# Optimization experiments

Hardware: AMD Instinct MI355X
Metric: run time of the kernel (lower is better)

## Reference

```python
import jax, jax.numpy as jnp
import numpy as np

BATCH = 32
N_LEVELS = (16384, 4096, 1024, 256)   # nodes at each mesh resolution
M_LEVELS = (4096, 1024, 256, 64)      # nodes after each Pool (downsample)
DEG = 6                               # directed edges per node
POOL_K = 3                            # nnz per row of downsample matrix
FILTERS = (3, 32, 32, 32, 64)         # channel chain of the 4 ChebConvs
K_CHEB = 6                            # Chebyshev polynomial order


def setup_inputs() -> dict:
    key = jax.random.key(0)
    ks = iter(jax.random.split(key, 64))
    inp = {"x": jax.random.normal(next(ks), (BATCH, N_LEVELS[0], FILTERS[0]), jnp.float32)}
    for i, N in enumerate(N_LEVELS):
        er = jnp.repeat(jnp.arange(N), DEG)
        off = jax.random.randint(next(ks), (N * DEG,), 1, N)
        inp[f"er{i}"] = er
        inp[f"ec{i}"] = (er + off) % N  # guaranteed no self loops
    for i, (M, N) in enumerate(zip(M_LEVELS, N_LEVELS)):
        inp[f"pr{i}"] = jnp.repeat(jnp.arange(M), POOL_K)
        inp[f"pc{i}"] = jax.random.randint(next(ks), (M * POOL_K,), 0, N)
        inp[f"pv{i}"] = jax.random.uniform(next(ks), (M * POOL_K,), jnp.float32)
    for i in range(4):
        fin, fout = FILTERS[i], FILTERS[i + 1]
        scale = 1.0 / np.sqrt(fin * K_CHEB)
        inp[f"W{i}"] = jax.random.normal(next(ks), (K_CHEB, fin, fout), jnp.float32) * scale
        inp[f"b{i}"] = jnp.zeros((fout,), jnp.float32)
    inp["enc_W"] = jax.random.normal(next(ks), (M_LEVELS[-1] * FILTERS[-1], 128), jnp.float32) * 0.1
    inp["enc_b"] = jnp.zeros((128,), jnp.float32)
    inp["cls_W"] = jax.random.normal(next(ks), (128, 10), jnp.float32) * 0.1
    inp["cls_b"] = jnp.zeros((10,), jnp.float32)
    return inp


def _cheb_conv(x, er, ec, W, b):
    # x: [B,N,Fin]; W: [K,Fin,Fout].
    # PyG ChebConv with lambda_max=2: L_hat = L - I = -D^{-1/2} A D^{-1/2}.
    N = x.shape[1]
    deg = jnp.zeros((N,), x.dtype).at[er].add(1.0)
    dinv = jnp.where(deg > 0, 1.0 / jnp.sqrt(jnp.maximum(deg, 1.0)), 0.0)
    norm = -(dinv[er] * dinv[ec])  # [E]

    def L(t):  # sparse matvec: gather neighbor feats, weight, scatter-add
        return jnp.zeros_like(t).at[:, er].add(t[:, ec] * norm[None, :, None])

    Tx0 = x
    out = jnp.einsum("bnf,fg->bng", Tx0, W[0])
    Tx1 = L(x)
    out = out + jnp.einsum("bnf,fg->bng", Tx1, W[1])
    for k in range(2, W.shape[0]):
        Tx2 = 2.0 * L(Tx1) - Tx0
        out = out + jnp.einsum("bnf,fg->bng", Tx2, W[k])
        Tx0, Tx1 = Tx1, Tx2
    return out + b


def _pool(x, pr, pc, pv, m):
    # sparse downsample matrix [m,N]: index_select cols * value, scatter_add rows
    B, _, F = x.shape
    return jnp.zeros((B, m, F), x.dtype).at[:, pr].add(x[:, pc] * pv[None, :, None])


def reference(x, er0, ec0, er1, ec1, er2, ec2, er3, ec3,
              pr0, pc0, pv0, pr1, pc1, pv1, pr2, pc2, pv2, pr3, pc3, pv3,
              W0, b0, W1, b1, W2, b2, W3, b3, enc_W, enc_b, cls_W, cls_b):
    ers, ecs = (er0, er1, er2, er3), (ec0, ec1, ec2, ec3)
    prs, pcs, pvs = (pr0, pr1, pr2, pr3), (pc0, pc1, pc2, pc3), (pv0, pv1, pv2, pv3)
    Ws, bs = (W0, W1, W2, W3), (b0, b1, b2, b3)
    for i in range(4):  # fixed n_layers loop (structurally distinct layers)
        x = jax.nn.relu(_cheb_conv(x, ers[i], ecs[i], Ws[i], bs[i]))
        x = _pool(x, prs[i], pcs[i], pvs[i], M_LEVELS[i])
    x = x.reshape(x.shape[0], -1)  # [B, 64*64]
    h = jax.nn.relu(x @ enc_W + enc_b)
    return h @ cls_W + cls_b
```

## Files before the change

### kernel.cpp

```cpp
#include <hip/hip_runtime.h>
#include <hip/hip_fp16.h>
#include <cstddef>
#include <cstdint>

#define BATCH 32


struct alignas(8) half4 { __half2 lo, hi; };

__device__ __forceinline__ void h4f(const half4 h, float f[4]) {
  float2 a = __half22float2(h.lo);
  float2 c = __half22float2(h.hi);
  f[0] = a.x; f[1] = a.y; f[2] = c.x; f[3] = c.y;
}
__device__ __forceinline__ void fma4(float4& a, float s, const float4& w) {
  a.x += s * w.x; a.y += s * w.y; a.z += s * w.z; a.w += s * w.w;
}
__device__ __forceinline__ float4 relu4(const float4& a) {
  return make_float4(fmaxf(a.x, 0.f), fmaxf(a.y, 0.f), fmaxf(a.z, 0.f), fmaxf(a.w, 0.f));
}

__global__ void __launch_bounds__(1024, 4) cheb_chain0(
    const float* __restrict__ x,
    const int* __restrict__ ec,
    __half* __restrict__ Th)
{
  __shared__ half4 cur[16384];
  const int b = blockIdx.x;
  const float cI = -1.0f / 6.0f;
  const float cS = -1.0f / 3.0f;
  half4 prevv[16];
  half4 newh[16];

#pragma unroll
  for (int i = 0; i < 16; ++i) {
    int n = threadIdx.x + (i << 10);
    const float* src = x + ((size_t)b * 16384 + n) * 3;
    half4 h;
    h.lo = __floats2half2_rn(src[0], src[1]);
    h.hi = __floats2half2_rn(src[2], 0.f);
    cur[n] = h;
  }
  __syncthreads();

#pragma unroll 1
  for (int k = 1; k <= 5; ++k) {
    half4* Tk = (half4*)Th + (size_t)(k - 1) * 524288 + (size_t)b * 16384;
#pragma unroll
    for (int i = 0; i < 16; ++i) {
      int n = threadIdx.x + (i << 10);
      const int2* e2 = (const int2*)(ec + n * 6);
      int2 ea = e2[0], eb = e2[1], ez = e2[2];
      int na[6];
      na[0] = ea.x; na[1] = ea.y; na[2] = eb.x;
      na[3] = eb.y; na[4] = ez.x; na[5] = ez.y;
      float s0 = 0.f, s1 = 0.f, s2 = 0.f;
#pragma unroll
      for (int d = 0; d < 6; ++d) {
        half4 t = cur[na[d]];
        float2 a = __half22float2(t.lo);
        float2 c = __half22float2(t.hi);
        s0 += a.x; s1 += a.y; s2 += c.x;
      }
      float v0, v1, v2;
      if (k == 1) {
        v0 = cI * s0; v1 = cI * s1; v2 = cI * s2;
      } else {
        float2 pa = __half22float2(prevv[i].lo);
        float2 pc = __half22float2(prevv[i].hi);
        v0 = cS * s0 - pa.x; v1 = cS * s1 - pa.y; v2 = cS * s2 - pc.x;
      }
      half4 h;
      h.lo = __floats2half2_rn(v0, v1);
      h.hi = __floats2half2_rn(v2, 0.f);
      newh[i] = h;
      Tk[n] = h;
    }
    __syncthreads();
#pragma unroll
    for (int i = 0; i < 16; ++i) {
      int n = threadIdx.x + (i << 10);
      prevv[i] = cur[n];
      cur[n] = newh[i];
    }
    __syncthreads();
  }
}

__global__ void __launch_bounds__(256) pool_conv_f3_bm(
    const float* __restrict__ x, const half4* __restrict__ T,
    const float* __restrict__ W, const float* __restrict__ bias,
    const int* __restrict__ pc, const float* __restrict__ pv,
    float* __restrict__ out)
{
  constexpr int FOUT = 32;
  constexpr int F4 = FOUT / 4;
  __shared__ float Ws[6 * 3 * FOUT];
  for (int i = threadIdx.x; i < 6 * 3 * FOUT; i += 256) Ws[i] = W[i];
  __syncthreads();
  const float4* Ws4 = (const float4*)Ws;
  int t = blockIdx.x * 256 + threadIdx.x;
  int fo4 = t % F4;
  int b   = (t / F4) % BATCH;
  int m   = t / (F4 * BATCH);
  int c0 = pc[m * 3 + 0], c1 = pc[m * 3 + 1], c2 = pc[m * 3 + 2];
  float v0 = pv[m * 3 + 0], v1 = pv[m * 3 + 1], v2 = pv[m * 3 + 2];
  float4 bi = ((const float4*)bias)[fo4];
  float4 a0 = bi, a1 = bi, a2 = bi;
  {
    const float* x0 = x + ((size_t)b * 16384 + c0) * 3;
    const float* x1 = x + ((size_t)b * 16384 + c1) * 3;
    const float* x2 = x + ((size_t)b * 16384 + c2) * 3;
#pragma unroll
    for (int f = 0; f < 3; ++f) {
      float4 w = Ws4[f * F4 + fo4];
      fma4(a0, x0[f], w);
      fma4(a1, x1[f], w);
      fma4(a2, x2[f], w);
    }
  }
#pragma unroll
  for (int k = 1; k < 6; ++k) {
    const half4* base = T + (size_t)(k - 1) * 524288 + (size_t)b * 16384;
    float r0[4], r1[4], r2[4];
    h4f(base[c0], r0);
    h4f(base[c1], r1);
    h4f(base[c2], r2);
#pragma unroll
    for (int f = 0; f < 3; ++f) {
      float4 w = Ws4[(k * 3 + f) * F4 + fo4];
      fma4(a0, r0[f], w);
      fma4(a1, r1[f], w);
      fma4(a2, r2[f], w);
    }
  }
  a0 = relu4(a0); a1 = relu4(a1); a2 = relu4(a2);
  float4 acc;
  acc.x = v0*a0.x + v1*a1.x + v2*a2.x;
  acc.y = v0*a0.y + v1*a1.y + v2*a2.y;
  acc.z = v0*a0.z + v1*a1.z + v2*a2.z;
  acc.w = v0*a0.w + v1*a1.w + v2*a2.w;
  ((float4*)out)[((size_t)m * BATCH + b) * F4 + fo4] = acc;
}

template<int N, int F, int THREADS, int MINW>
__global__ void __launch_bounds__(THREADS, MINW) cheb_recur_hh(
    const float* __restrict__ X,
    const int* __restrict__ ec,
    __half* __restrict__ Th)
{
  constexpr int NPT = N / THREADS;
  __shared__ half4 cur[N];
  const float cI = -1.0f / 6.0f;
  const float cS = -1.0f / 3.0f;
  const int b = blockIdx.x & 31;
  const int fbase = (blockIdx.x >> 5) * 4;
  constexpr size_t SLH = (size_t)N * 32 * F;
  half4 prevv[NPT];
  half4 newh[NPT];
#pragma unroll
  for (int i = 0; i < NPT; ++i) {
    int n = threadIdx.x + i * THREADS;
    float4 xv = *(const float4*)(X + ((size_t)n * 32 + b) * F + fbase);
    half4 h;
    h.lo = __floats2half2_rn(xv.x, xv.y);
    h.hi = __floats2half2_rn(xv.z, xv.w);
    cur[n] = h;
  }
  __syncthreads();
#pragma unroll 1
  for (int k = 1; k <= 5; ++k) {
    __half* Tk = Th + (size_t)(k - 1) * SLH;
#pragma unroll
    for (int i = 0; i < NPT; ++i) {
      int n = threadIdx.x + i * THREADS;
      const int2* e2 = (const int2*)(ec + n * 6);
      int2 ea = e2[0], eb = e2[1], ez = e2[2];
      int na[6];
      na[0] = ea.x; na[1] = ea.y; na[2] = eb.x;
      na[3] = eb.y; na[4] = ez.x; na[5] = ez.y;
      float s0 = 0.f, s1 = 0.f, s2 = 0.f, s3 = 0.f;
#pragma unroll
      for (int d = 0; d < 6; ++d) {
        half4 t = cur[na[d]];
        float2 a = __half22float2(t.lo);
        float2 c = __half22float2(t.hi);
        s0 += a.x; s1 += a.y; s2 += c.x; s3 += c.y;
      }
      float v0, v1, v2, v3;
      if (k == 1) {
        v0 = cI * s0; v1 = cI * s1; v2 = cI * s2; v3 = cI * s3;
      } else {
        float2 pa = __half22float2(prevv[i].lo);
        float2 pc = __half22float2(prevv[i].hi);
        v0 = cS * s0 - pa.x; v1 = cS * s1 - pa.y;
        v2 = cS * s2 - pc.x; v3 = cS * s3 - pc.y;
      }
      half4 h;
      h.lo = __floats2half2_rn(v0, v1);
      h.hi = __floats2half2_rn(v2, v3);
      newh[i] = h;
      *(half4*)(Tk + ((size_t)n * 32 + b) * F + fbase) = h;
    }
    __syncthreads();
#pragma unroll
    for (int i = 0; i < NPT; ++i) {
      int n = threadIdx.x + i * THREADS;
      prevv[i] = cur[n];
      cur[n] = newh[i];
    }
    __syncthreads();
  }
}

template<int N, int M, int FOUT, bool OUT_BM>
__global__ void __launch_bounds__(256) pool_conv_v32_h(
    const float* __restrict__ X, const __half* __restrict__ Th,
    const float* __restrict__ W, const float* __restrict__ bias,
    const int* __restrict__ pc, const float* __restrict__ pv,
    float* __restrict__ out)
{
  constexpr int FIN = 32;
  constexpr int F4 = FOUT / 4;
  constexpr size_t SLH = (size_t)N * 32 * FIN;
  __shared__ float Ws[6 * FIN * FOUT];
  for (int i = threadIdx.x; i < 6 * FIN * FOUT; i += 256) Ws[i] = W[i];
  __syncthreads();
  const float4* Ws4 = (const float4*)Ws;
  const float4* X4p = (const float4*)X;
  int t = blockIdx.x * 256 + threadIdx.x;
  int fo4 = t % F4;
  int b   = (t / F4) % BATCH;
  int m   = t / (F4 * BATCH);
  int c0 = pc[m * 3 + 0], c1 = pc[m * 3 + 1], c2 = pc[m * 3 + 2];
  float v0 = pv[m * 3 + 0], v1 = pv[m * 3 + 1], v2 = pv[m * 3 + 2];
  float4 bi = ((const float4*)bias)[fo4];
  float4 a0 = bi, a1 = bi, a2 = bi;
  {
    const float4* r0 = X4p + ((size_t)c0 * BATCH + b) * 8;
    const float4* r1 = X4p + ((size_t)c1 * BATCH + b) * 8;
    const float4* r2 = X4p + ((size_t)c2 * BATCH + b) * 8;
#pragma unroll
    for (int fi = 0; fi < 8; ++fi) {
      float4 t0 = r0[fi], t1 = r1[fi], t2 = r2[fi];
#pragma unroll
      for (int ff = 0; ff < 4; ++ff) {
        float4 w = Ws4[(fi * 4 + ff) * F4 + fo4];
        fma4(a0, ((const float*)&t0)[ff], w);
        fma4(a1, ((const float*)&t1)[ff], w);
        fma4(a2, ((const float*)&t2)[ff], w);
      }
    }
  }
#pragma unroll 1
  for (int k = 1; k < 6; ++k) {
    const half4* base = (const half4*)(Th + (size_t)(k - 1) * SLH);
    const half4* r0 = base + ((size_t)c0 * 32 + b) * 8;
    const half4* r1 = base + ((size_t)c1 * 32 + b) * 8;
    const half4* r2 = base + ((size_t)c2 * 32 + b) * 8;
#pragma unroll
    for (int q = 0; q < 8; ++q) {
      float f0[4], f1[4], f2[4];
      h4f(r0[q], f0); h4f(r1[q], f1); h4f(r2[q], f2);
#pragma unroll
      for (int ff = 0; ff < 4; ++ff) {
        float4 w = Ws4[((k * 32) + q * 4 + ff) * F4 + fo4];
        fma4(a0, f0[ff], w);
        fma4(a1, f1[ff], w);
        fma4(a2, f2[ff], w);
      }
    }
  }
  a0 = relu4(a0); a1 = relu4(a1); a2 = relu4(a2);
  float4 acc;
  acc.x = v0*a0.x + v1*a1.x + v2*a2.x;
  acc.y = v0*a0.y + v1*a1.y + v2*a2.y;
  acc.z = v0*a0.z + v1*a1.z + v2*a2.z;
  acc.w = v0*a0.w + v1*a1.w + v2*a2.w;
  size_t oi = OUT_BM ? (((size_t)b * M + m) * F4 + fo4) : (((size_t)m * BATCH + b) * F4 + fo4);
  ((float4*)out)[oi] = acc;
}

__global__ void __launch_bounds__(256) encoder_partial(
    const float* __restrict__ Xf, const float* __restrict__ encW,
    float* __restrict__ partial)
{
  int b  = blockIdx.x;
  int ks = blockIdx.y;
  int fo = threadIdx.x & 127;
  int half = threadIdx.x >> 7;
  const float* xr = Xf + b * 4096 + ks * 256 + half * 128;
  const float* w  = encW + (size_t)(ks * 256 + half * 128) * 128;
  float acc = 0.f;
#pragma unroll 8
  for (int i = 0; i < 128; ++i) acc += xr[i] * w[(size_t)i * 128 + fo];
  __shared__ float part[256];
  part[threadIdx.x] = acc;
  __syncthreads();
  if (half == 0) partial[(size_t)(b * 16 + ks) * 128 + fo] = part[fo] + part[128 + fo];
}

__global__ void __launch_bounds__(128) encoder_reduce_cls(
    const float* __restrict__ partial, const float* __restrict__ encB,
    const float* __restrict__ clsW, const float* __restrict__ clsB,
    float* __restrict__ out)
{
  int b = blockIdx.x;
  int fo = threadIdx.x;
  float acc = encB[fo];
#pragma unroll
  for (int ks = 0; ks < 16; ++ks) acc += partial[(size_t)(b * 16 + ks) * 128 + fo];
  __shared__ float Hs[128];
  Hs[fo] = fmaxf(acc, 0.f);
  __syncthreads();
  if (fo < 10) {
    float s = clsB[fo];
#pragma unroll 4
    for (int f = 0; f < 128; ++f) s += Hs[f] * clsW[f * 10 + fo];
    out[b * 10 + fo] = s;
  }
}

extern "C" void kernel_launch(void* const* d_in, const int* in_sizes, int n_in,
                              void* d_out, int out_size, void* d_ws, size_t ws_size,
                              hipStream_t stream)
{
  const float* x   = (const float*)d_in[0];
  const int* ec0 = (const int*)d_in[2];
  const int* ec1 = (const int*)d_in[4];
  const int* ec2 = (const int*)d_in[6];
  const int* ec3 = (const int*)d_in[8];
  const int* pc0 = (const int*)d_in[10]; const float* pv0 = (const float*)d_in[11];
  const int* pc1 = (const int*)d_in[13]; const float* pv1 = (const float*)d_in[14];
  const int* pc2 = (const int*)d_in[16]; const float* pv2 = (const float*)d_in[17];
  const int* pc3 = (const int*)d_in[19]; const float* pv3 = (const float*)d_in[20];
  const float* W0 = (const float*)d_in[21]; const float* b0 = (const float*)d_in[22];
  const float* W1 = (const float*)d_in[23]; const float* b1 = (const float*)d_in[24];
  const float* W2 = (const float*)d_in[25]; const float* b2 = (const float*)d_in[26];
  const float* W3 = (const float*)d_in[27]; const float* b3 = (const float*)d_in[28];
  const float* encW = (const float*)d_in[29]; const float* encB = (const float*)d_in[30];
  const float* clsW = (const float*)d_in[31]; const float* clsB = (const float*)d_in[32];
  float* out = (float*)d_out;

  float* ws = (float*)d_ws;
  __half* Th = (__half*)ws;
  float* X1 = ws + 10485760;
  float* X2 = X1 + 4194304;
  float* X3 = X2 + 1048576;
  float* X4 = X3 + 262144;
  float* P  = X4 + 131072;

  dim3 blk(256);

  cheb_chain0<<<dim3(32), dim3(1024), 0, stream>>>(x, ec0, Th);
  pool_conv_f3_bm<<<dim3(4096), blk, 0, stream>>>(
      x, (const half4*)Th, W0, b0, pc0, pv0, X1);

  cheb_recur_hh<4096, 32, 1024, 4><<<dim3(256), dim3(1024), 0, stream>>>(X1, ec1, Th);
  pool_conv_v32_h<4096, 1024, 32, false><<<dim3(1024), blk, 0, stream>>>(
      X1, Th, W1, b1, pc1, pv1, X2);

  cheb_recur_hh<1024, 32, 256, 4><<<dim3(256), blk, 0, stream>>>(X2, ec2, Th);
  pool_conv_v32_h<1024, 256, 32, false><<<dim3(256), blk, 0, stream>>>(
      X2, Th, W2, b2, pc2, pv2, X3);

  cheb_recur_hh<256, 32, 256, 4><<<dim3(256), blk, 0, stream>>>(X3, ec3, Th);
  pool_conv_v32_h<256, 64, 64, true><<<dim3(128), blk, 0, stream>>>(
      X3, Th, W3, b3, pc3, pv3, X4);

  encoder_partial<<<dim3(32, 16), blk, 0, stream>>>(X4, encW, P);
  encoder_reduce_cls<<<dim3(32), dim3(128), 0, stream>>>(P, encB, clsW, clsB, out);
}
```

Before: 346.4 us.

## Fuse whole network into cooperative mega-kernel and spread level-0 recurrence across grid

Replaces the chain of separate launches with a single cooperative kernel that uses grid-wide syncs between stages. The level-0 Chebyshev recurrence, previously run by 32 blocks in shared memory, is now distributed over all blocks with a node-major half-precision layout in global memory. The aim is to remove launch gaps and the low parallelism of the first layer. In exchange it adds grid-sync overhead and global-memory round trips between recurrence steps, and falls back to multi-kernel launches if the cooperative launch fails.

After: 726.1 us. 2.1x slower.

```diff
diff --git a/kernel.cpp b/kernel.cpp
--- a/kernel.cpp
+++ b/kernel.cpp
@@ -1,7 +1,10 @@
 #include <hip/hip_runtime.h>
 #include <hip/hip_fp16.h>
+#include <hip/hip_cooperative_groups.h>
 #include <cstddef>
 #include <cstdint>
+
+namespace cg = cooperative_groups;
 
 #define BATCH 32
 
@@ -20,86 +23,99 @@
   return make_float4(fmaxf(a.x, 0.f), fmaxf(a.y, 0.f), fmaxf(a.z, 0.f), fmaxf(a.w, 0.f));
 }
 
-__global__ void __launch_bounds__(1024, 4) cheb_chain0(
-    const float* __restrict__ x,
-    const int* __restrict__ ec,
-    __half* __restrict__ Th)
-{
-  __shared__ half4 cur[16384];
-  const int b = blockIdx.x;
-  const float cI = -1.0f / 6.0f;
-  const float cS = -1.0f / 3.0f;
-  half4 prevv[16];
-  half4 newh[16];
-
-#pragma unroll
-  for (int i = 0; i < 16; ++i) {
-    int n = threadIdx.x + (i << 10);
-    const float* src = x + ((size_t)b * 16384 + n) * 3;
-    half4 h;
-    h.lo = __floats2half2_rn(src[0], src[1]);
-    h.hi = __floats2half2_rn(src[2], 0.f);
-    cur[n] = h;
-  }
-  __syncthreads();
-
-#pragma unroll 1
-  for (int k = 1; k <= 5; ++k) {
-    half4* Tk = (half4*)Th + (size_t)(k - 1) * 524288 + (size_t)b * 16384;
-#pragma unroll
-    for (int i = 0; i < 16; ++i) {
-      int n = threadIdx.x + (i << 10);
-      const int2* e2 = (const int2*)(ec + n * 6);
-      int2 ea = e2[0], eb = e2[1], ez = e2[2];
-      int na[6];
-      na[0] = ea.x; na[1] = ea.y; na[2] = eb.x;
-      na[3] = eb.y; na[4] = ez.x; na[5] = ez.y;
-      float s0 = 0.f, s1 = 0.f, s2 = 0.f;
-#pragma unroll
-      for (int d = 0; d < 6; ++d) {
-        half4 t = cur[na[d]];
-        float2 a = __half22float2(t.lo);
-        float2 c = __half22float2(t.hi);
-        s0 += a.x; s1 += a.y; s2 += c.x;
-      }
-      float v0, v1, v2;
-      if (k == 1) {
-        v0 = cI * s0; v1 = cI * s1; v2 = cI * s2;
-      } else {
-        float2 pa = __half22float2(prevv[i].lo);
-        float2 pc = __half22float2(prevv[i].hi);
-        v0 = cS * s0 - pa.x; v1 = cS * s1 - pa.y; v2 = cS * s2 - pc.x;
-      }
-      half4 h;
-      h.lo = __floats2half2_rn(v0, v1);
-      h.hi = __floats2half2_rn(v2, 0.f);
-      newh[i] = h;
-      Tk[n] = h;
-    }
-    __syncthreads();
-#pragma unroll
-    for (int i = 0; i < 16; ++i) {
-      int n = threadIdx.x + (i << 10);
-      prevv[i] = cur[n];
-      cur[n] = newh[i];
-    }
-    __syncthreads();
-  }
-}
-
-__global__ void __launch_bounds__(256) pool_conv_f3_bm(
-    const float* __restrict__ x, const half4* __restrict__ T,
-    const float* __restrict__ W, const float* __restrict__ bias,
+
+__device__ __forceinline__ void d_transpose_cell(
+    const float* __restrict__ x, half4* __restrict__ xh, int t)
+{
+  int n = t >> 5;
+  int b = t & 31;
+  const float* src = x + ((size_t)b * 16384 + n) * 3;
+  half4 h;
+  h.lo = __floats2half2_rn(src[0], src[1]);
+  h.hi = __floats2half2_rn(src[2], 0.f);
+  xh[t] = h;
+}
+
+__device__ __forceinline__ void d_cheb_cell(
+    const half4* __restrict__ Tin, const half4* __restrict__ Tpp,
+    const int* __restrict__ ec, half4* __restrict__ Tout,
+    float coef, float beta, int idx)
+{
+  int n = idx >> 5;
+  const int2* e2 = (const int2*)(ec + n * 6);
+  int2 ea = e2[0], eb = e2[1], ez = e2[2];
+  int na[6];
+  na[0] = ea.x; na[1] = ea.y; na[2] = eb.x;
+  na[3] = eb.y; na[4] = ez.x; na[5] = ez.y;
+  int b = idx & 31;
+  float s0 = 0.f, s1 = 0.f, s2 = 0.f;
+#pragma unroll
+  for (int d = 0; d < 6; ++d) {
+    half4 v = Tin[(na[d] << 5) | b];
+    float2 a = __half22float2(v.lo);
+    float2 c = __half22float2(v.hi);
+    s0 += a.x; s1 += a.y; s2 += c.x;
+  }
+  half4 p = Tpp[idx];
+  float2 pa = __half22float2(p.lo);
+  float2 pc = __half22float2(p.hi);
+  half4 o;
+  o.lo = __floats2half2_rn(coef * s0 + beta * pa.x, coef * s1 + beta * pa.y);
+  o.hi = __floats2half2_rn(coef * s2 + beta * pc.x, 0.f);
+  Tout[idx] = o;
+}
+
+__device__ __forceinline__ void d_poolf3_cell(
+    const half4* __restrict__ Xh, const half4* __restrict__ T,
+    const float* __restrict__ Ws, const float* __restrict__ bias,
     const int* __restrict__ pc, const float* __restrict__ pv,
-    float* __restrict__ out)
-{
-  constexpr int FOUT = 32;
+    float* __restrict__ out, int t)
+{
+  constexpr int F4 = 8;
+  constexpr size_t SL = (size_t)16384 * 32;
+  const float4* Ws4 = (const float4*)Ws;
+  int fo4 = t % F4;
+  int b   = (t / F4) % BATCH;
+  int m   = t / (F4 * BATCH);
+  int c0 = pc[m * 3 + 0], c1 = pc[m * 3 + 1], c2 = pc[m * 3 + 2];
+  float v0 = pv[m * 3 + 0], v1 = pv[m * 3 + 1], v2 = pv[m * 3 + 2];
+  float4 bi = ((const float4*)bias)[fo4];
+  float4 a0 = bi, a1 = bi, a2 = bi;
+#pragma unroll
+  for (int k = 0; k < 6; ++k) {
+    const half4* base = (k == 0) ? Xh : (T + (size_t)(k - 1) * SL);
+    float r0[4], r1[4], r2[4];
+    h4f(base[(c0 << 5) | b], r0);
+    h4f(base[(c1 << 5) | b], r1);
+    h4f(base[(c2 << 5) | b], r2);
+#pragma unroll
+    for (int f = 0; f < 3; ++f) {
+      float4 w = Ws4[(k * 3 + f) * F4 + fo4];
+      fma4(a0, r0[f], w);
+      fma4(a1, r1[f], w);
+      fma4(a2, r2[f], w);
+    }
+  }
+  a0 = relu4(a0); a1 = relu4(a1); a2 = relu4(a2);
+  float4 acc;
+  acc.x = v0*a0.x + v1*a1.x + v2*a2.x;
+  acc.y = v0*a0.y + v1*a1.y + v2*a2.y;
+  acc.z = v0*a0.z + v1*a1.z + v2*a2.z;
+  acc.w = v0*a0.w + v1*a1.w + v2*a2.w;
+  ((float4*)out)[((size_t)m * BATCH + b) * F4 + fo4] = acc;
+}
+
+template<int N, int M, int FOUT, bool OUT_BM>
+__device__ __forceinline__ void d_pool32_cell(
+    const float* __restrict__ X, const __half* __restrict__ Th,
+    const float* __restrict__ Ws, const float* __restrict__ bias,
+    const int* __restrict__ pc, const float* __restrict__ pv,
+    float* __restrict__ out, int t)
+{
   constexpr int F4 = FOUT / 4;
-  __shared__ float Ws[6 * 3 * FOUT];
-  for (int i = threadIdx.x; i < 6 * 3 * FOUT; i += 256) Ws[i] = W[i];
-  __syncthreads();
+  constexpr size_t SLH = (size_t)N * 32 * 32;
   const float4* Ws4 = (const float4*)Ws;
-  int t = blockIdx.x * 256 + threadIdx.x;
+  const float4* X4p = (const float4*)X;
   int fo4 = t % F4;
   int b   = (t / F4) % BATCH;
   int m   = t / (F4 * BATCH);
@@ -108,30 +124,38 @@
   float4 bi = ((const float4*)bias)[fo4];
   float4 a0 = bi, a1 = bi, a2 = bi;
   {
-    const float* x0 = x + ((size_t)b * 16384 + c0) * 3;
-    const float* x1 = x + ((size_t)b * 16384 + c1) * 3;
-    const float* x2 = x + ((size_t)b * 16384 + c2) * 3;
-#pragma unroll
-    for (int f = 0; f < 3; ++f) {
-      float4 w = Ws4[f * F4 + fo4];
-      fma4(a0, x0[f], w);
-      fma4(a1, x1[f], w);
-      fma4(a2, x2[f], w);
-    }
-  }
-#pragma unroll
+    const float4* r0 = X4p + ((size_t)c0 * BATCH + b) * 8;
+    const float4* r1 = X4p + ((size_t)c1 * BATCH + b) * 8;
+    const float4* r2 = X4p + ((size_t)c2 * BATCH + b) * 8;
+#pragma unroll
+    for (int fi = 0; fi < 8; ++fi) {
+      float4 t0 = r0[fi], t1 = r1[fi], t2 = r2[fi];
+#pragma unroll
+      for (int ff = 0; ff < 4; ++ff) {
+        float4 w = Ws4[(fi * 4 + ff) * F4 + fo4];
+        fma4(a0, ((const float*)&t0)[ff], w);
+        fma4(a1, ((const float*)&t1)[ff], w);
+        fma4(a2, ((const float*)&t2)[ff], w);
+      }
+    }
+  }
+#pragma unroll 1
   for (int k = 1; k < 6; ++k) {
-    const half4* base = T + (size_t)(k - 1) * 524288 + (size_t)b * 16384;
-    float r0[4], r1[4], r2[4];
-    h4f(base[c0], r0);
-    h4f(base[c1], r1);
-    h4f(base[c2], r2);
-#pragma unroll
-    for (int f = 0; f < 3; ++f) {
-      float4 w = Ws4[(k * 3 + f) * F4 + fo4];
-      fma4(a0, r0[f], w);
-      fma4(a1, r1[f], w);
-      fma4(a2, r2[f], w);
+    const half4* base = (const half4*)(Th + (size_t)(k - 1) * SLH);
+    const half4* r0 = base + ((size_t)c0 * 32 + b) * 8;
+    const half4* r1 = base + ((size_t)c1 * 32 + b) * 8;
+    const half4* r2 = base + ((size_t)c2 * 32 + b) * 8;
+#pragma unroll
+    for (int q = 0; q < 8; ++q) {
+      float f0[4], f1[4], f2[4];
+      h4f(r0[q], f0); h4f(r1[q], f1); h4f(r2[q], f2);
+#pragma unroll
+      for (int ff = 0; ff < 4; ++ff) {
+        float4 w = Ws4[((k * 32) + q * 4 + ff) * F4 + fo4];
+        fma4(a0, f0[ff], w);
+        fma4(a1, f1[ff], w);
+        fma4(a2, f2[ff], w);
+      }
     }
   }
   a0 = relu4(a0); a1 = relu4(a1); a2 = relu4(a2);
@@ -140,13 +164,240 @@
   acc.y = v0*a0.y + v1*a1.y + v2*a2.y;
   acc.z = v0*a0.z + v1*a1.z + v2*a2.z;
   acc.w = v0*a0.w + v1*a1.w + v2*a2.w;
-  ((float4*)out)[((size_t)m * BATCH + b) * F4 + fo4] = acc;
+  size_t oi = OUT_BM ? (((size_t)b * M + m) * F4 + fo4) : (((size_t)m * BATCH + b) * F4 + fo4);
+  ((float4*)out)[oi] = acc;
+}
+
+template<int N, int NPT>
+__device__ void d_recur_stage(
+    const float* __restrict__ X, const int* __restrict__ ec,
+    __half* __restrict__ Th, half4* cur, int bid, int tid)
+{
+  const float cI = -1.0f / 6.0f;
+  const float cS = -1.0f / 3.0f;
+  const int b = bid & 31;
+  const int fbase = (bid >> 5) * 4;
+  constexpr size_t SLH = (size_t)N * 32 * 32;
+  half4 prevv[NPT], newh[NPT];
+#pragma unroll
+  for (int i = 0; i < NPT; ++i) {
+    int n = tid + i * 512;
+    if (n < N) {
+      float4 xv = *(const float4*)(X + ((size_t)n * 32 + b) * 32 + fbase);
+      half4 h;
+      h.lo = __floats2half2_rn(xv.x, xv.y);
+      h.hi = __floats2half2_rn(xv.z, xv.w);
+      cur[n] = h;
+    }
+  }
+  __syncthreads();
+#pragma unroll 1
+  for (int k = 1; k <= 5; ++k) {
+    __half* Tk = Th + (size_t)(k - 1) * SLH;
+#pragma unroll
+    for (int i = 0; i < NPT; ++i) {
+      int n = tid + i * 512;
+      if (n < N) {
+        const int2* e2 = (const int2*)(ec + n * 6);
+        int2 ea = e2[0], eb = e2[1], ez = e2[2];
+        int na[6];
+        na[0] = ea.x; na[1] = ea.y; na[2] = eb.x;
+        na[3] = eb.y; na[4] = ez.x; na[5] = ez.y;
+        float s0 = 0.f, s1 = 0.f, s2 = 0.f, s3 = 0.f;
+#pragma unroll
+        for (int d = 0; d < 6; ++d) {
+          half4 t = cur[na[d]];
+          float2 a = __half22float2(t.lo);
+          float2 c = __half22float2(t.hi);
+          s0 += a.x; s1 += a.y; s2 += c.x; s3 += c.y;
+        }
+        float v0, v1, v2, v3;
+        if (k == 1) {
+          v0 = cI * s0; v1 = cI * s1; v2 = cI * s2; v3 = cI * s3;
+        } else {
+          float2 pa = __half22float2(prevv[i].lo);
+          float2 pc = __half22float2(prevv[i].hi);
+          v0 = cS * s0 - pa.x; v1 = cS * s1 - pa.y;
+          v2 = cS * s2 - pc.x; v3 = cS * s3 - pc.y;
+        }
+        half4 h;
+        h.lo = __floats2half2_rn(v0, v1);
+        h.hi = __floats2half2_rn(v2, v3);
+        newh[i] = h;
+        *(half4*)(Tk + ((size_t)n * 32 + b) * 32 + fbase) = h;
+      }
+    }
+    __syncthreads();
+#pragma unroll
+    for (int i = 0; i < NPT; ++i) {
+      int n = tid + i * 512;
+      if (n < N) {
+        prevv[i] = cur[n];
+        cur[n] = newh[i];
+      }
+    }
+    __syncthreads();
+  }
+}
+
+
+struct MegaP {
+  const float* x;
+  const int *ec0, *ec1, *ec2, *ec3;
+  const int *pc0, *pc1, *pc2, *pc3;
+  const float *pv0, *pv1, *pv2, *pv3;
+  const float *W0, *b0, *W1, *b1, *W2, *b2, *W3, *b3;
+  const float *encW, *encB, *clsW, *clsB;
+  float* out;
+  half4* Xh; __half* Th;
+  float *X1, *X2, *X3, *X4, *P;
+};
+
+__global__ void __launch_bounds__(512, 2) mega(MegaP P)
+{
+  cg::grid_group grid = cg::this_grid();
+  __shared__ __align__(16) char smemraw[49152];
+  half4* scur = (half4*)smemraw;
+  float* sws  = (float*)smemraw;
+  const int bid = blockIdx.x;
+  const int tid = threadIdx.x;
+  const float cI = -1.0f / 6.0f;
+  const float cS = -1.0f / 3.0f;
+
+#pragma unroll
+  for (int u = 0; u < 4; ++u)
+    d_transpose_cell(P.x, P.Xh, u * 131072 + bid * 512 + tid);
+  grid.sync();
+
+  {
+    const size_t S = (size_t)16384 * 32;
+    half4* T4 = (half4*)P.Th;
+    const half4* Tin[5] = { P.Xh, T4, T4 + S, T4 + 2*S, T4 + 3*S };
+    const half4* Tpp[5] = { P.Xh, P.Xh, T4, T4 + S, T4 + 2*S };
+    half4* Tout[5]      = { T4, T4 + S, T4 + 2*S, T4 + 3*S, T4 + 4*S };
+#pragma unroll 1
+    for (int k = 0; k < 5; ++k) {
+      float coef = (k == 0) ? cI : cS;
+      float beta = (k == 0) ? 0.f : -1.f;
+#pragma unroll
+      for (int u = 0; u < 4; ++u)
+        d_cheb_cell(Tin[k], Tpp[k], P.ec0, Tout[k], coef, beta,
+                    u * 131072 + bid * 512 + tid);
+      grid.sync();
+    }
+  }
+
+  for (int i = tid; i < 6 * 3 * 32; i += 512) sws[i] = P.W0[i];
+  __syncthreads();
+#pragma unroll 1
+  for (int u = 0; u < 8; ++u)
+    d_poolf3_cell(P.Xh, (const half4*)P.Th, sws, P.b0, P.pc0, P.pv0, P.X1,
+                  u * 131072 + bid * 512 + tid);
+  grid.sync();
+
+  d_recur_stage<4096, 8>(P.X1, P.ec1, P.Th, scur, bid, tid);
+  grid.sync();
+
+  for (int i = tid; i < 6 * 32 * 32; i += 512) sws[i] = P.W1[i];
+  __syncthreads();
+#pragma unroll 1
+  for (int u = 0; u < 2; ++u)
+    d_pool32_cell<4096, 1024, 32, false>(P.X1, P.Th, sws, P.b1, P.pc1, P.pv1,
+                                         P.X2, u * 131072 + bid * 512 + tid);
+  grid.sync();
+
+  d_recur_stage<1024, 2>(P.X2, P.ec2, P.Th, scur, bid, tid);
+  grid.sync();
+
+  for (int i = tid; i < 6 * 32 * 32; i += 512) sws[i] = P.W2[i];
+  __syncthreads();
+  {
+    int t = bid * 512 + tid;
+    if (t < 65536)
+      d_pool32_cell<1024, 256, 32, false>(P.X2, P.Th, sws, P.b2, P.pc2, P.pv2,
+                                          P.X3, t);
+  }
+  grid.sync();
+
+  d_recur_stage<256, 1>(P.X3, P.ec3, P.Th, scur, bid, tid);
+  grid.sync();
+
+  for (int i = tid; i < 6 * 32 * 64; i += 512) sws[i] = P.W3[i];
+  __syncthreads();
+  {
+    int t = bid * 512 + tid;
+    if (t < 32768)
+      d_pool32_cell<256, 64, 64, true>(P.X3, P.Th, sws, P.b3, P.pc3, P.pv3,
+                                       P.X4, t);
+  }
+  grid.sync();
+
+  {
+    int t = bid * 512 + tid;
+    if (t < 65536) {
+      int fo = t & 127;
+      int ks = (t >> 7) & 15;
+      int b  = t >> 11;
+      const float* xr = P.X4 + b * 4096 + ks * 256;
+      const float* w  = P.encW + (size_t)(ks * 256) * 128 + fo;
+      float acc = 0.f;
+#pragma unroll 8
+      for (int i = 0; i < 256; ++i) acc += xr[i] * w[(size_t)i * 128];
+      P.P[(size_t)(b * 16 + ks) * 128 + fo] = acc;
+    }
+  }
+  grid.sync();
+
+  if (bid < 32) {
+    int b = bid;
+    float* hs = sws;
+    if (tid < 128) {
+      float acc = P.encB[tid];
+#pragma unroll
+      for (int ks = 0; ks < 16; ++ks)
+        acc += P.P[(size_t)(b * 16 + ks) * 128 + tid];
+      hs[tid] = fmaxf(acc, 0.f);
+    }
+    __syncthreads();
+    if (tid < 10) {
+      float s = P.clsB[tid];
+#pragma unroll 4
+      for (int f = 0; f < 128; ++f) s += hs[f] * P.clsW[f * 10 + tid];
+      P.out[b * 10 + tid] = s;
+    }
+  }
+}
+
+
+__global__ void __launch_bounds__(256) transpose_h(
+    const float* __restrict__ x, half4* __restrict__ xh)
+{
+  d_transpose_cell(x, xh, blockIdx.x * 256 + threadIdx.x);
+}
+
+__global__ void __launch_bounds__(256) cheb_step_h(
+    const half4* __restrict__ Tin, const half4* __restrict__ Tpp,
+    const int* __restrict__ ec, half4* __restrict__ Tout,
+    float coef, float beta)
+{
+  d_cheb_cell(Tin, Tpp, ec, Tout, coef, beta, blockIdx.x * 256 + threadIdx.x);
+}
+
+__global__ void __launch_bounds__(256) pool_conv_f3_h(
+    const half4* __restrict__ Xh, const half4* __restrict__ T,
+    const float* __restrict__ W, const float* __restrict__ bias,
+    const int* __restrict__ pc, const float* __restrict__ pv,
+    float* __restrict__ out)
+{
+  __shared__ float Ws[6 * 3 * 32];
+  for (int i = threadIdx.x; i < 6 * 3 * 32; i += 256) Ws[i] = W[i];
+  __syncthreads();
+  d_poolf3_cell(Xh, T, Ws, bias, pc, pv, out, blockIdx.x * 256 + threadIdx.x);
 }
 
 template<int N, int F, int THREADS, int MINW>
 __global__ void __launch_bounds__(THREADS, MINW) cheb_recur_hh(
-    const float* __restrict__ X,
-    const int* __restrict__ ec,
+    const float* __restrict__ X, const int* __restrict__ ec,
     __half* __restrict__ Th)
 {
   constexpr int NPT = N / THREADS;
@@ -156,8 +407,7 @@
   const int b = blockIdx.x & 31;
   const int fbase = (blockIdx.x >> 5) * 4;
   constexpr size_t SLH = (size_t)N * 32 * F;
-  half4 prevv[NPT];
-  half4 newh[NPT];
+  half4 prevv[NPT], newh[NPT];
 #pragma unroll
   for (int i = 0; i < NPT; ++i) {
     int n = threadIdx.x + i * THREADS;
@@ -220,65 +470,11 @@
     const int* __restrict__ pc, const float* __restrict__ pv,
     float* __restrict__ out)
 {
-  constexpr int FIN = 32;
-  constexpr int F4 = FOUT / 4;
-  constexpr size_t SLH = (size_t)N * 32 * FIN;
-  __shared__ float Ws[6 * FIN * FOUT];
-  for (int i = threadIdx.x; i < 6 * FIN * FOUT; i += 256) Ws[i] = W[i];
-  __syncthreads();
-  const float4* Ws4 = (const float4*)Ws;
-  const float4* X4p = (const float4*)X;
-  int t = blockIdx.x * 256 + threadIdx.x;
-  int fo4 = t % F4;
-  int b   = (t / F4) % BATCH;
-  int m   = t / (F4 * BATCH);
-  int c0 = pc[m * 3 + 0], c1 = pc[m * 3 + 1], c2 = pc[m * 3 + 2];
-  float v0 = pv[m * 3 + 0], v1 = pv[m * 3 + 1], v2 = pv[m * 3 + 2];
-  float4 bi = ((const float4*)bias)[fo4];
-  float4 a0 = bi, a1 = bi, a2 = bi;
-  {
-    const float4* r0 = X4p + ((size_t)c0 * BATCH + b) * 8;
-    const float4* r1 = X4p + ((size_t)c1 * BATCH + b) * 8;
-    const float4* r2 = X4p + ((size_t)c2 * BATCH + b) * 8;
-#pragma unroll
-    for (int fi = 0; fi < 8; ++fi) {
-      float4 t0 = r0[fi], t1 = r1[fi], t2 = r2[fi];
-#pragma unroll
-      for (int ff = 0; ff < 4; ++ff) {
-        float4 w = Ws4[(fi * 4 + ff) * F4 + fo4];
-        fma4(a0, ((const float*)&t0)[ff], w);
-        fma4(a1, ((const float*)&t1)[ff], w);
-        fma4(a2, ((const float*)&t2)[ff], w);
-      }
-    }
-  }
-#pragma unroll 1
-  for (int k = 1; k < 6; ++k) {
-    const half4* base = (const half4*)(Th + (size_t)(k - 1) * SLH);
-    const half4* r0 = base + ((size_t)c0 * 32 + b) * 8;
-    const half4* r1 = base + ((size_t)c1 * 32 + b) * 8;
-    const half4* r2 = base + ((size_t)c2 * 32 + b) * 8;
-#pragma unroll
-    for (int q = 0; q < 8; ++q) {
-      float f0[4], f1[4], f2[4];
-      h4f(r0[q], f0); h4f(r1[q], f1); h4f(r2[q], f2);
-#pragma unroll
-      for (int ff = 0; ff < 4; ++ff) {
-        float4 w = Ws4[((k * 32) + q * 4 + ff) * F4 + fo4];
-        fma4(a0, f0[ff], w);
-        fma4(a1, f1[ff], w);
-        fma4(a2, f2[ff], w);
-      }
-    }
-  }
-  a0 = relu4(a0); a1 = relu4(a1); a2 = relu4(a2);
-  float4 acc;
-  acc.x = v0*a0.x + v1*a1.x + v2*a2.x;
-  acc.y = v0*a0.y + v1*a1.y + v2*a2.y;
-  acc.z = v0*a0.z + v1*a1.z + v2*a2.z;
-  acc.w = v0*a0.w + v1*a1.w + v2*a2.w;
-  size_t oi = OUT_BM ? (((size_t)b * M + m) * F4 + fo4) : (((size_t)m * BATCH + b) * F4 + fo4);
-  ((float4*)out)[oi] = acc;
+  __shared__ float Ws[6 * 32 * FOUT];
+  for (int i = threadIdx.x; i < 6 * 32 * FOUT; i += 256) Ws[i] = W[i];
+  __syncthreads();
+  d_pool32_cell<N, M, FOUT, OUT_BM>(X, Th, Ws, bias, pc, pv, out,
+                                    blockIdx.x * 256 + threadIdx.x);
 }
 
 __global__ void __launch_bounds__(256) encoder_partial(
@@ -320,6 +516,7 @@
     out[b * 10 + fo] = s;
   }
 }
+
 
 extern "C" void kernel_launch(void* const* d_in, const int* in_sizes, int n_in,
                               void* d_out, int out_size, void* d_ws, size_t ws_size,
@@ -343,31 +540,56 @@
   float* out = (float*)d_out;
 
   float* ws = (float*)d_ws;
-  __half* Th = (__half*)ws;
-  float* X1 = ws + 10485760;
+  half4*  Xh = (half4*)ws;
+  __half* Th = (__half*)(ws + 1048576);
+  float* X1 = ws + 1048576 + 10485760;
   float* X2 = X1 + 4194304;
   float* X3 = X2 + 1048576;
   float* X4 = X3 + 262144;
   float* P  = X4 + 131072;
 
-  dim3 blk(256);
-
-  cheb_chain0<<<dim3(32), dim3(1024), 0, stream>>>(x, ec0, Th);
-  pool_conv_f3_bm<<<dim3(4096), blk, 0, stream>>>(
-      x, (const half4*)Th, W0, b0, pc0, pv0, X1);
-
-  cheb_recur_hh<4096, 32, 1024, 4><<<dim3(256), dim3(1024), 0, stream>>>(X1, ec1, Th);
-  pool_conv_v32_h<4096, 1024, 32, false><<<dim3(1024), blk, 0, stream>>>(
-      X1, Th, W1, b1, pc1, pv1, X2);
-
-  cheb_recur_hh<1024, 32, 256, 4><<<dim3(256), blk, 0, stream>>>(X2, ec2, Th);
-  pool_conv_v32_h<1024, 256, 32, false><<<dim3(256), blk, 0, stream>>>(
-      X2, Th, W2, b2, pc2, pv2, X3);
-
-  cheb_recur_hh<256, 32, 256, 4><<<dim3(256), blk, 0, stream>>>(X3, ec3, Th);
-  pool_conv_v32_h<256, 64, 64, true><<<dim3(128), blk, 0, stream>>>(
-      X3, Th, W3, b3, pc3, pv3, X4);
-
-  encoder_partial<<<dim3(32, 16), blk, 0, stream>>>(X4, encW, P);
-  encoder_reduce_cls<<<dim3(32), dim3(128), 0, stream>>>(P, encB, clsW, clsB, out);
-}
+  MegaP mp;
+  mp.x = x;
+  mp.ec0 = ec0; mp.ec1 = ec1; mp.ec2 = ec2; mp.ec3 = ec3;
+  mp.pc0 = pc0; mp.pc1 = pc1; mp.pc2 = pc2; mp.pc3 = pc3;
+  mp.pv0 = pv0; mp.pv1 = pv1; mp.pv2 = pv2; mp.pv3 = pv3;
+  mp.W0 = W0; mp.b0 = b0; mp.W1 = W1; mp.b1 = b1;
+  mp.W2 = W2; mp.b2 = b2; mp.W3 = W3; mp.b3 = b3;
+  mp.encW = encW; mp.encB = encB; mp.clsW = clsW; mp.clsB = clsB;
+  mp.out = out;
+  mp.Xh = Xh; mp.Th = Th;
+  mp.X1 = X1; mp.X2 = X2; mp.X3 = X3; mp.X4 = X4; mp.P = P;
+
+  void* kargs[] = { (void*)&mp };
+  hipError_t e = hipLaunchCooperativeKernel((const void*)mega, dim3(256), dim3(512),
+                                            kargs, 0, stream);
+  if (e != hipSuccess) {
+    (void)hipGetLastError();
+    const float cI = -1.0f / 6.0f;
+    const float cS = -1.0f / 3.0f;
+    dim3 blk(256);
+    transpose_h<<<dim3(2048), blk, 0, stream>>>(x, Xh);
+    {
+      constexpr size_t S = (size_t)16384 * 32;
+      half4* T4 = (half4*)Th;
+      cheb_step_h<<<dim3(2048), blk, 0, stream>>>(Xh,       Xh,       ec0, T4,        cI,  0.f);
+      cheb_step_h<<<dim3(2048), blk, 0, stream>>>(T4,       Xh,       ec0, T4 + S,    cS, -1.f);
+      cheb_step_h<<<dim3(2048), blk, 0, stream>>>(T4 + S,   T4,       ec0, T4 + 2*S,  cS, -1.f);
+      cheb_step_h<<<dim3(2048), blk, 0, stream>>>(T4 + 2*S, T4 + S,   ec0, T4 + 3*S,  cS, -1.f);
+      cheb_step_h<<<dim3(2048), blk, 0, stream>>>(T4 + 3*S, T4 + 2*S, ec0, T4 + 4*S,  cS, -1.f);
+      pool_conv_f3_h<<<dim3(4096), blk, 0, stream>>>(
+          Xh, (const half4*)Th, W0, b0, pc0, pv0, X1);
+    }
+    cheb_recur_hh<4096, 32, 1024, 4><<<dim3(256), dim3(1024), 0, stream>>>(X1, ec1, Th);
+    pool_conv_v32_h<4096, 1024, 32, false><<<dim3(1024), blk, 0, stream>>>(
+        X1, Th, W1, b1, pc1, pv1, X2);
+    cheb_recur_hh<1024, 32, 256, 4><<<dim3(256), blk, 0, stream>>>(X2, ec2, Th);
+    pool_conv_v32_h<1024, 256, 32, false><<<dim3(256), blk, 0, stream>>>(
+        X2, Th, W2, b2, pc2, pv2, X3);
+    cheb_recur_hh<256, 32, 256, 4><<<dim3(256), blk, 0, stream>>>(X3, ec3, Th);
+    pool_conv_v32_h<256, 64, 64, true><<<dim3(128), blk, 0, stream>>>(
+        X3, Th, W3, b3, pc3, pv3, X4);
+    encoder_partial<<<dim3(32, 16), blk, 0, stream>>>(X4, encW, P);
+    encoder_reduce_cls<<<dim3(32), dim3(128), 0, stream>>>(P, encB, clsW, clsB, out);
+  }
+}
```
